# Performance work log

Hardware: AMD Instinct MI355X
Metric: run time of the kernel (lower is better)

## Reference

```python
import jax, jax.numpy as jnp
import numpy as np

N, F, E, A, H = 50000, 64, 1600000, 8, 16
RECEPTIVE_FIELD = 7


def setup_inputs() -> dict:
    key = jax.random.key(0)
    ks = jax.random.split(key, 12)
    inp = {
        "x": jax.random.normal(ks[0], (N, F), dtype=jnp.float32),
        "edge_index": jax.random.randint(ks[1], (2, E), 0, N, dtype=jnp.int64),
        "w1": jax.random.normal(ks[2], (F, H), dtype=jnp.float32) * 0.1,
        "b1": jax.random.normal(ks[3], (H,), dtype=jnp.float32) * 0.1,
        "w2": jax.random.normal(ks[4], (H, H), dtype=jnp.float32) * 0.1,
        "b2": jax.random.normal(ks[5], (H,), dtype=jnp.float32) * 0.1,
        "w3": jax.random.normal(ks[6], (H, F), dtype=jnp.float32) * 0.1,
        "b3": jax.random.normal(ks[7], (F,), dtype=jnp.float32) * 0.1,
        "fc1_w": jax.random.normal(ks[8], ((1 + RECEPTIVE_FIELD) * F, F), dtype=jnp.float32) * 0.05,
        "fc1_b": jax.random.normal(ks[9], (F,), dtype=jnp.float32) * 0.05,
        "fc2_w": jax.random.normal(ks[10], (F, A), dtype=jnp.float32) * 0.1,
        "fc2_b": jax.random.normal(ks[11], (A,), dtype=jnp.float32) * 0.1,
    }
    return inp


def _mlp(x, w1, b1, w2, b2, w3, b3):
    h = jax.nn.relu(x @ w1 + b1)
    h = jax.nn.relu(h @ w2 + b2)
    return h @ w3 + b3


def _agg_mean(x, src, dst):
    # scatter-mean: mean of source-node features over incoming edges per target
    s = jax.ops.segment_sum(x[src], dst, num_segments=N)          # [N, F]
    cnt = jax.ops.segment_sum(jnp.ones((src.shape[0], 1), x.dtype), dst, num_segments=N)
    return s / jnp.maximum(cnt, 1.0)  # nodes with no in-edges -> 0 (torch mean aggr)


def reference(x, edge_index, w1, b1, w2, b2, w3, b3, fc1_w, fc1_b, fc2_w, fc2_b):
    src, dst = edge_index[0], edge_index[1]
    mlp = lambda t: _mlp(t, w1, b1, w2, b2, w3, b3)
    fields = [mlp(mlp(x))]
    for i in range(RECEPTIVE_FIELD):
        x_ = mlp(x)
        for _ in range(i + 1):
            x_ = _agg_mean(x_, src, dst)
        fields.append(mlp(x_))
    f = jnp.concatenate(fields, axis=1)          # [N, 8*F]
    h = f @ fc1_w + fc1_b                        # [N, F]
    logits = h @ fc2_w + fc2_b                   # [N, A]
    return jax.nn.softmax(logits, axis=-1)       # Categorical probs
```

## Files before the change

kernel.cpp:

```cpp
#include <hip/hip_runtime.h>


#define NB2MAX 400
#define NBLK   256
#define CAP2   32
#define CAPC   48
#define CAPB   6144
#define OVCAP  1024
#define LCAP   6144
#define CAPN   64

__global__ __launch_bounds__(1024) void binfill_k(
    const int* __restrict__ src, const int* __restrict__ dst, int E, int n,
    int* __restrict__ gcur, int* __restrict__ ovbuf,
    int* __restrict__ bins, int* __restrict__ cnts,
    const float* __restrict__ w1, const float* __restrict__ w3,
    const float* __restrict__ b3, const float* __restrict__ fc1w,
    const float* __restrict__ fc1b, const float* __restrict__ fc2w,
    const float* __restrict__ fc2b,
    float* __restrict__ M, float* __restrict__ cvec,
    float* __restrict__ W31, float* __restrict__ c31) {
    __shared__ int lbuf[NB2MAX * CAP2];
    __shared__ int lcnt[NB2MAX];
    __shared__ int lflush[NB2MAX];
    int tid = threadIdx.x;
    int NB = (n + 127) >> 7;

    if ((int)blockIdx.x >= NBLK) {
        float* fl = (float*)lbuf;
        int s = (int)blockIdx.x - NBLK;
        if (s == 0) {
            if (tid < 256) {
                int i = tid >> 4, j = tid & 15;
                float a = 0.f;
                for (int g = 0; g < 64; g++) a += w3[i * 64 + g] * w1[g * 16 + j];
                W31[tid] = a;
            } else if (tid < 272) {
                int j = tid - 256;
                float a = 0.f;
                for (int g = 0; g < 64; g++) a += b3[g] * w1[g * 16 + j];
                c31[j] = a;
            } else if (tid >= 320 && tid < 384) {
                int h = tid - 320;
                float a = 0.f;
                for (int r = 0; r < 512; r++) a += b3[r & 63] * fc1w[r * 64 + h];
                fl[h] = a;
            }
            __syncthreads();
            if (tid < 8) {
                float a = fc2b[tid];
                for (int h = 0; h < 64; h++) a += (fc1b[h] + fl[h]) * fc2w[h * 8 + tid];
                cvec[tid] = a;
            }
        } else {
            int k = s - 1;
            {
                int i = tid >> 6, h = tid & 63;
                float a = 0.f;
                const float* f1 = fc1w + (size_t)(k * 64) * 64 + h;
                for (int g = 0; g < 64; g++) a += w3[i * 64 + g] * f1[g * 64];
                fl[i * 64 + h] = a;
            }
            __syncthreads();
            if (tid < 128) {
                int i = tid >> 3, j = tid & 7;
                float a = 0.f;
                for (int h = 0; h < 64; h++) a += fl[i * 64 + h] * fc2w[h * 8 + j];
                M[k * 128 + i * 8 + j] = a;
            }
        }
        return;
    }

    for (int b = tid; b < NB; b += 1024) { lcnt[b] = 0; lflush[b] = 0; }
    __syncthreads();
    int blk = blockIdx.x;
    int chunk = (E + NBLK - 1) / NBLK;
    int beg = blk * chunk;
    int end = beg + chunk; if (end > E) end = E;
    for (int t0 = beg; t0 < end; t0 += 1024) {
        int e = t0 + tid;
        if (e < end) {
            int d = dst[e], s = src[e];
            if ((unsigned)d < (unsigned)n && (unsigned)s < (unsigned)n) {
                int b = d >> 7;
                int pk = ((d & 127) << 16) | s;
                int pos = atomicAdd(&lcnt[b], 1);
                if (pos < CAP2) lbuf[b * CAP2 + pos] = pk;
                else {
                    int p = atomicAdd(&gcur[b], 1);
                    if (p < OVCAP) ovbuf[b * OVCAP + p] = pk;
                }
            }
        }
        __syncthreads();
        for (int b = tid; b < NB; b += 1024) {
            int cnt = lcnt[b]; if (cnt > CAP2) cnt = CAP2;
            int fl2 = lflush[b];
            size_t cell = ((size_t)b * NBLK + blk) * CAPC;
            int base = 0;
            while (cnt - base >= 16) {
                if (fl2 + 16 <= CAPC) {
                    int* dp = bins + cell + fl2;
                    #pragma unroll
                    for (int q = 0; q < 16; q++) dp[q] = lbuf[b * CAP2 + base + q];
                    fl2 += 16;
                } else {
                    int p = atomicAdd(&gcur[b], 16);
                    for (int q = 0; q < 16; q++)
                        if (p + q < OVCAP) ovbuf[b * OVCAP + p + q] = lbuf[b * CAP2 + base + q];
                }
                base += 16;
            }
            int rem = cnt - base;
            if (base > 0)
                for (int q = 0; q < rem; q++) lbuf[b * CAP2 + q] = lbuf[b * CAP2 + base + q];
            lcnt[b] = rem; lflush[b] = fl2;
        }
        __syncthreads();
    }
    for (int b = tid; b < NB; b += 1024) {
        int cnt = lcnt[b]; if (cnt > CAP2) cnt = CAP2;
        int fl2 = lflush[b];
        size_t cell = ((size_t)b * NBLK + blk) * CAPC;
        if (fl2 + cnt <= CAPC) {
            for (int q = 0; q < cnt; q++) bins[cell + fl2 + q] = lbuf[b * CAP2 + q];
            fl2 += cnt;
        } else {
            int p = atomicAdd(&gcur[b], cnt);
            for (int q = 0; q < cnt; q++)
                if (p + q < OVCAP) ovbuf[b * OVCAP + p + q] = lbuf[b * CAP2 + q];
        }
        cnts[(size_t)blk * NB + b] = fl2;
    }
}

__global__ __launch_bounds__(256) void csr2_k(
    const int* __restrict__ bins, const int* __restrict__ cnts,
    const int* __restrict__ gcur, const int* __restrict__ ovbuf,
    unsigned short* __restrict__ csrp, int* __restrict__ degs,
    int* __restrict__ csr, int2* __restrict__ be,
    int* __restrict__ lists, int* __restrict__ lcnt3, int n) {
    __shared__ int hist[128], pref[128], cur[128];
    __shared__ int scnt[NBLK];
    __shared__ int lbuf[LCAP];
    __shared__ int sov;
    __shared__ int ccnt[3], cbase[3];
    int tid = threadIdx.x;
    int NB = (n + 127) >> 7;
    int b = blockIdx.x;
    if (tid < 128) { hist[tid] = 0; cur[tid] = 0; }
    if (tid < 3) ccnt[tid] = 0;
    scnt[tid] = cnts[(size_t)tid * NB + b];
    if (tid == 0) {
        int g = gcur[b];
        sov = g < 0 ? 0 : (g > OVCAP ? OVCAP : g);
    }
    __syncthreads();
    {
        int c = scnt[tid];
        size_t cell = ((size_t)b * NBLK + tid) * CAPC;
        for (int i = 0; i < c; i++) atomicAdd(&hist[bins[cell + i] >> 16], 1);
    }
    if (tid == 0)
        for (int i = 0; i < sov; i++) atomicAdd(&hist[ovbuf[b * OVCAP + i] >> 16], 1);
    __syncthreads();
    if (tid == 0) {
        int r = 0;
        for (int i = 0; i < 128; i++) { pref[i] = r; r += hist[i]; }
    }
    __syncthreads();
    {
        int c = scnt[tid];
        size_t cell = ((size_t)b * NBLK + tid) * CAPC;
        for (int i = 0; i < c; i++) {
            int pk = bins[cell + i];
            int dl = pk >> 16;
            int pos = pref[dl] + atomicAdd(&cur[dl], 1);
            if (pos < LCAP) lbuf[pos] = pk & 0xffff;
        }
    }
    if (tid == 0) {
        for (int i = 0; i < sov; i++) {
            int pk = ovbuf[b * OVCAP + i];
            int dl = pk >> 16;
            int pos = pref[dl] + atomicAdd(&cur[dl], 1);
            if (pos < LCAP) lbuf[pos] = pk & 0xffff;
        }
    }
    __syncthreads();
    for (int q = tid; q < 128 * CAPN; q += 256) {
        int dl = q >> 6, j = q & 63;
        int d = (b << 7) + dl;
        if (d >= n) break;
        int cnt = hist[dl];
        int v = (j < cnt) ? lbuf[pref[dl] + j] : n;
        int pos = ((j & 3) << 4) | (j >> 2);
        csrp[(size_t)d * CAPN + pos] = (unsigned short)v;
    }
    int myc = -1, lpos = 0;
    if (tid < 128) {
        int d = (b << 7) + tid;
        if (d < n) {
            int cnt = hist[tid];
            degs[d] = cnt;
            myc = cnt <= 32 ? 0 : (cnt <= 48 ? 1 : 2);
            lpos = atomicAdd(&ccnt[myc], 1);
            if (cnt > CAPN) {
                int s0 = b * CAPB + pref[tid];
                be[d] = make_int2(s0 + CAPN, s0 + cnt);
                for (int j = CAPN; j < cnt; j++)
                    csr[s0 + j] = lbuf[pref[tid] + j] << 2;
            }
        }
    }
    __syncthreads();
    if (tid < 3) cbase[tid] = atomicAdd(&lcnt3[tid], ccnt[tid]);
    __syncthreads();
    if (myc >= 0) lists[(size_t)myc * n + cbase[myc] + lpos] = (b << 7) + tid;
}

__global__ __launch_bounds__(256) void proj_k(
    const float* __restrict__ x, float* __restrict__ z0, float* __restrict__ z1,
    float* __restrict__ logits,
    const float* __restrict__ w1, const float* __restrict__ b1,
    const float* __restrict__ w2, const float* __restrict__ b2,
    const float* __restrict__ W31, const float* __restrict__ c31,
    const float* __restrict__ M0, const float* __restrict__ cvec, int n) {
    __shared__ float sw1[1024], sw2[256], sW[256], sM[128];
    __shared__ float sb1[16], sb2[16], sc[16], scv[8];
    int tid = threadIdx.x;
    for (int i = tid; i < 1024; i += 256) sw1[i] = w1[i];
    sw2[tid] = w2[tid & 255];
    sW[tid & 255] = W31[tid & 255];
    if (tid < 128) sM[tid] = M0[tid];
    if (tid < 16) { sb1[tid] = b1[tid]; sb2[tid] = b2[tid]; sc[tid] = c31[tid]; }
    if (tid < 8) scv[tid] = cvec[tid];
    __syncthreads();
    if (blockIdx.x == 0 && tid < 16) {
        z0[(size_t)n * 16 + tid] = 0.f;
        z1[(size_t)n * 16 + tid] = 0.f;
    }
    int nid = blockIdx.x * 256 + tid;
    if (nid >= n) return;
    float t1[16];
    #pragma unroll
    for (int j = 0; j < 16; j++) t1[j] = sb1[j];
    const float4* xp = (const float4*)(x + (size_t)nid * 64);
    #pragma unroll
    for (int q = 0; q < 16; q++) {
        float4 v = xp[q];
        #pragma unroll
        for (int j = 0; j < 16; j++)
            t1[j] += v.x * sw1[(4 * q) * 16 + j] + v.y * sw1[(4 * q + 1) * 16 + j]
                   + v.z * sw1[(4 * q + 2) * 16 + j] + v.w * sw1[(4 * q + 3) * 16 + j];
    }
    #pragma unroll
    for (int j = 0; j < 16; j++) t1[j] = fmaxf(t1[j], 0.f);
    float t2[16];
    #pragma unroll
    for (int j = 0; j < 16; j++) {
        float a = sb2[j];
        #pragma unroll
        for (int i = 0; i < 16; i++) a += t1[i] * sw2[i * 16 + j];
        t2[j] = fmaxf(a, 0.f);
    }
    float z[16];
    #pragma unroll
    for (int j = 0; j < 16; j++) {
        float a = sc[j];
        #pragma unroll
        for (int i = 0; i < 16; i++) a += t2[i] * sW[i * 16 + j];
        z[j] = a;
    }
    float4* zo = (float4*)(z0 + (size_t)nid * 16);
    #pragma unroll
    for (int q = 0; q < 4; q++)
        zo[q] = make_float4(z[4 * q], z[4 * q + 1], z[4 * q + 2], z[4 * q + 3]);
    float h[16], f2[16];
    #pragma unroll
    for (int i = 0; i < 16; i++) h[i] = fmaxf(z[i] + sb1[i], 0.f);
    #pragma unroll
    for (int j = 0; j < 16; j++) {
        float a = sb2[j];
        #pragma unroll
        for (int i = 0; i < 16; i++) a += h[i] * sw2[i * 16 + j];
        f2[j] = fmaxf(a, 0.f);
    }
    float* lp = logits + (size_t)nid * 8;
    #pragma unroll
    for (int j = 0; j < 8; j++) {
        float l = scv[j];
        #pragma unroll
        for (int i = 0; i < 16; i++) l += f2[i] * sM[i * 8 + j];
        lp[j] = l;
    }
}

__global__ __launch_bounds__(256, 4) void hop_k(
    const float* __restrict__ zin, float* __restrict__ zout, float* __restrict__ logits,
    const unsigned short* __restrict__ csrp, const int* __restrict__ degs,
    const int2* __restrict__ be, const int* __restrict__ csr,
    const int* __restrict__ lists, const int* __restrict__ lcnt3,
    const float* __restrict__ w2, const float* __restrict__ b1,
    const float* __restrict__ b2, const float* __restrict__ M, int n, int FB) {
    __shared__ float sw2[256], sM[128], sb1[16], sb2[16];
    int tid = threadIdx.x;
    if ((int)blockIdx.x < FB) {
        sw2[tid] = w2[tid];
        if (tid < 128) sM[tid] = M[tid];
        if (tid < 16) { sb1[tid] = b1[tid]; sb2[tid] = b2[tid]; }
        __syncthreads();
        int nid = blockIdx.x * 256 + tid;
        if (nid >= n) return;
        float h[16];
        const float4* zp = (const float4*)(zin + (size_t)nid * 16);
        #pragma unroll
        for (int q = 0; q < 4; q++) {
            float4 v = zp[q];
            h[4 * q] = v.x; h[4 * q + 1] = v.y; h[4 * q + 2] = v.z; h[4 * q + 3] = v.w;
        }
        #pragma unroll
        for (int i = 0; i < 16; i++) h[i] = fmaxf(h[i] + sb1[i], 0.f);
        float t2[16];
        #pragma unroll
        for (int j = 0; j < 16; j++) {
            float a = sb2[j];
            #pragma unroll
            for (int i = 0; i < 16; i++) a += h[i] * sw2[i * 16 + j];
            t2[j] = fmaxf(a, 0.f);
        }
        float* lp = logits + (size_t)nid * 8;
        #pragma unroll
        for (int j = 0; j < 8; j++) {
            float l = 0.f;
            #pragma unroll
            for (int i = 0; i < 16; i++) l += t2[i] * sM[i * 8 + j];
            lp[j] += l;
        }
        return;
    }
    int wave = tid >> 6;
    int lane = tid & 63;
    int quarter = lane >> 4;
    int l16 = lane & 15;
    int t = l16 >> 2, c = l16 & 3;
    int idx = (((int)blockIdx.x - FB) * 4 + wave) * 4 + quarter;
    if (idx >= n) return;
    int ns = lcnt3[0];
    int nm = lcnt3[1];
    int tier, node;
    if (idx < ns)           { tier = 0; node = lists[idx]; }
    else if (idx < ns + nm) { tier = 1; node = lists[(size_t)n + (idx - ns)]; }
    else                    { tier = 2; node = lists[2 * (size_t)n + (idx - ns - nm)]; }
    int degi = degs[node];
    const uint4* ip = (const uint4*)(csrp + ((size_t)node << 6));
    uint4 pa = ip[t * 2];
    int r0 = pa.x & 0xffff, r1 = pa.x >> 16;
    int r2 = pa.y & 0xffff, r3 = pa.y >> 16;
    int r4 = pa.z & 0xffff, r5 = pa.z >> 16;
    int r6 = pa.w & 0xffff, r7 = pa.w >> 16;
    const float4* z4 = (const float4*)zin;
    float4 v0 = z4[((size_t)r0 << 2) + c];
    float4 v1 = z4[((size_t)r1 << 2) + c];
    float4 v2 = z4[((size_t)r2 << 2) + c];
    float4 v3 = z4[((size_t)r3 << 2) + c];
    float4 v4 = z4[((size_t)r4 << 2) + c];
    float4 v5 = z4[((size_t)r5 << 2) + c];
    float4 v6 = z4[((size_t)r6 << 2) + c];
    float4 v7 = z4[((size_t)r7 << 2) + c];
    float ax = ((v0.x + v1.x) + (v2.x + v3.x)) + ((v4.x + v5.x) + (v6.x + v7.x));
    float ay = ((v0.y + v1.y) + (v2.y + v3.y)) + ((v4.y + v5.y) + (v6.y + v7.y));
    float az = ((v0.z + v1.z) + (v2.z + v3.z)) + ((v4.z + v5.z) + (v6.z + v7.z));
    float aw = ((v0.w + v1.w) + (v2.w + v3.w)) + ((v4.w + v5.w) + (v6.w + v7.w));
    if (tier >= 1) {
        uint4 pb = ip[t * 2 + 1];
        int r8 = pb.x & 0xffff, r9 = pb.x >> 16;
        int rA = pb.y & 0xffff, rB = pb.y >> 16;
        float4 v8 = z4[((size_t)r8 << 2) + c];
        float4 v9 = z4[((size_t)r9 << 2) + c];
        float4 vA = z4[((size_t)rA << 2) + c];
        float4 vB = z4[((size_t)rB << 2) + c];
        ax += (v8.x + v9.x) + (vA.x + vB.x);
        ay += (v8.y + v9.y) + (vA.y + vB.y);
        az += (v8.z + v9.z) + (vA.z + vB.z);
        aw += (v8.w + v9.w) + (vA.w + vB.w);
        if (tier == 2) {
            int rC = pb.z & 0xffff, rD = pb.z >> 16;
            int rE = pb.w & 0xffff, rF = pb.w >> 16;
            float4 vC = z4[((size_t)rC << 2) + c];
            float4 vD = z4[((size_t)rD << 2) + c];
            float4 vE = z4[((size_t)rE << 2) + c];
            float4 vF = z4[((size_t)rF << 2) + c];
            ax += (vC.x + vD.x) + (vE.x + vF.x);
            ay += (vC.y + vD.y) + (vE.y + vF.y);
            az += (vC.z + vD.z) + (vE.z + vF.z);
            aw += (vC.w + vD.w) + (vE.w + vF.w);
            if (degi > CAPN) {
                int2 r = be[node];
                for (int q = r.x + t; q < r.y; q += 4) {
                    float4 v = z4[(size_t)csr[q] + c];
                    ax += v.x; ay += v.y; az += v.z; aw += v.w;
                }
            }
        }
    }
    #pragma unroll
    for (int off = 8; off >= 4; off >>= 1) {
        ax += __shfl_down(ax, off, 16);
        ay += __shfl_down(ay, off, 16);
        az += __shfl_down(az, off, 16);
        aw += __shfl_down(aw, off, 16);
    }
    if (l16 < 4) {
        float inv = 1.f / (float)(degi > 0 ? degi : 1);
        ((float4*)(zout + (size_t)node * 16))[l16] =
            make_float4(ax * inv, ay * inv, az * inv, aw * inv);
    }
}

__global__ __launch_bounds__(256) void fieldsoft_k(
    const float* __restrict__ z, float* __restrict__ logits,
    const float* __restrict__ w2, const float* __restrict__ b1,
    const float* __restrict__ b2, const float* __restrict__ M, int n) {
    __shared__ float sw2[256], sM[128], sb1[16], sb2[16];
    int tid = threadIdx.x;
    sw2[tid] = w2[tid];
    if (tid < 128) sM[tid] = M[tid];
    if (tid < 16) { sb1[tid] = b1[tid]; sb2[tid] = b2[tid]; }
    __syncthreads();
    int nid = blockIdx.x * 256 + tid;
    if (nid >= n) return;
    float h[16];
    const float4* zp = (const float4*)(z + (size_t)nid * 16);
    #pragma unroll
    for (int q = 0; q < 4; q++) {
        float4 v = zp[q];
        h[4 * q] = v.x; h[4 * q + 1] = v.y; h[4 * q + 2] = v.z; h[4 * q + 3] = v.w;
    }
    #pragma unroll
    for (int i = 0; i < 16; i++) h[i] = fmaxf(h[i] + sb1[i], 0.f);
    float t2[16];
    #pragma unroll
    for (int j = 0; j < 16; j++) {
        float a = sb2[j];
        #pragma unroll
        for (int i = 0; i < 16; i++) a += h[i] * sw2[i * 16 + j];
        t2[j] = fmaxf(a, 0.f);
    }
    float4* lp4 = (float4*)(logits + (size_t)nid * 8);
    float4 l0 = lp4[0], l1 = lp4[1];
    float v[8] = {l0.x, l0.y, l0.z, l0.w, l1.x, l1.y, l1.z, l1.w};
    #pragma unroll
    for (int j = 0; j < 8; j++) {
        float l = 0.f;
        #pragma unroll
        for (int i = 0; i < 16; i++) l += t2[i] * sM[i * 8 + j];
        v[j] += l;
    }
    float m = v[0];
    #pragma unroll
    for (int j = 1; j < 8; j++) m = fmaxf(m, v[j]);
    float s = 0.f;
    #pragma unroll
    for (int j = 0; j < 8; j++) { v[j] = expf(v[j] - m); s += v[j]; }
    float inv = 1.f / s;
    lp4[0] = make_float4(v[0] * inv, v[1] * inv, v[2] * inv, v[3] * inv);
    lp4[1] = make_float4(v[4] * inv, v[5] * inv, v[6] * inv, v[7] * inv);
}

extern "C" void kernel_launch(void* const* d_in, const int* in_sizes, int n_in,
                              void* d_out, int out_size, void* d_ws, size_t ws_size,
                              hipStream_t stream) {
    const float* x    = (const float*)d_in[0];
    const int*   ei   = (const int*)d_in[1];
    const float* w1   = (const float*)d_in[2];
    const float* b1   = (const float*)d_in[3];
    const float* w2   = (const float*)d_in[4];
    const float* b2   = (const float*)d_in[5];
    const float* w3   = (const float*)d_in[6];
    const float* b3   = (const float*)d_in[7];
    const float* fc1w = (const float*)d_in[8];
    const float* fc1b = (const float*)d_in[9];
    const float* fc2w = (const float*)d_in[10];
    const float* fc2b = (const float*)d_in[11];
    float* out = (float*)d_out;

    int n = in_sizes[0] / 64;
    int E = in_sizes[1] / 2;
    int NB = (n + 127) >> 7;
    const int* src = ei;
    const int* dst = ei + E;

    char* ws = (char*)d_ws;
    auto carve = [&](size_t bytes) {
        char* p = ws;
        ws += (bytes + 255) & ~((size_t)255);
        return p;
    };
    int*   gcur    = (int*)carve((size_t)NB * 4);
    int*   lcnt3   = (int*)carve(16);
    int*   ovbuf   = (int*)carve((size_t)NB * OVCAP * 4);
    int*   binsbuf = (int*)carve((size_t)NB * NBLK * CAPC * 4);
    int*   cnts    = (int*)carve((size_t)NBLK * NB * 4);
    unsigned short* csrp = (unsigned short*)carve((size_t)n * CAPN * 2);
    int*   degs    = (int*)carve((size_t)n * 4);
    int*   csr     = (int*)carve((size_t)NB * CAPB * 4);
    int2*  be      = (int2*)carve((size_t)n * 8);
    int*   lists   = (int*)carve((size_t)3 * n * 4);
    float* buf0    = (float*)carve((size_t)(n + 1) * 16 * 4);
    float* buf1    = (float*)carve((size_t)(n + 1) * 16 * 4);
    float* M       = (float*)carve(1024 * 4);
    float* cvec    = (float*)carve(8 * 4);
    float* W31     = (float*)carve(256 * 4);
    float* c31     = (float*)carve(16 * 4);

    size_t gpad = ((size_t)NB * 4 + 255) & ~((size_t)255);
    hipMemsetAsync(gcur, 0, gpad + 16, stream);
    binfill_k<<<NBLK + 9, 1024, 0, stream>>>(src, dst, E, n, gcur, ovbuf, binsbuf, cnts,
                                             w1, w3, b3, fc1w, fc1b, fc2w, fc2b,
                                             M, cvec, W31, c31);

    int FB = (n + 255) / 256;
    int AB = (n + 15) / 16;
    csr2_k<<<NB, 256, 0, stream>>>(binsbuf, cnts, gcur, ovbuf, csrp, degs, csr, be,
                                   lists, lcnt3, n);
    proj_k<<<FB, 256, 0, stream>>>(x, buf0, buf1, out, w1, b1, w2, b2,
                                   W31, c31, M, cvec, n);

    float* cur = buf0;
    float* nxt = buf1;
    hop_k<<<AB, 256, 0, stream>>>(cur, nxt, out, csrp, degs, be, csr, lists, lcnt3,
                                  w2, b1, b2, M, n, 0);
    { float* t = cur; cur = nxt; nxt = t; }
    for (int k = 1; k <= 6; k++) {
        hop_k<<<FB + AB, 256, 0, stream>>>(cur, nxt, out, csrp, degs, be, csr,
                                           lists, lcnt3,
                                           w2, b1, b2, M + k * 128, n, FB);
        float* t = cur; cur = nxt; nxt = t;
    }
    fieldsoft_k<<<FB, 256, 0, stream>>>(cur, out, w2, b1, b2, M + 7 * 128, n);
}
```

Before: 255.2 us.

## Fuse projection and seven aggregation hops into one cooperative persistent kernel

Replaces the projection kernel, the seven hop launches and the final field-softmax kernel with a single cooperative kernel of 512 blocks. Grid-wide syncs separate the hops, and each thread keeps its node's logits in registers until the final softmax, so the per-hop read-modify-write of logits in global memory goes away. The aim is to cut launch overhead and logits traffic. The cost is a fixed small grid with low occupancy for the latency-bound gathers, plus per-hop serialization of aggregation and MLP work that the separate launches could partly overlap. It falls back to the old multi-kernel path when the stream is being captured or the cooperative launch fails.

```diff
diff --git a/kernel.cpp b/kernel.cpp
--- a/kernel.cpp
+++ b/kernel.cpp
@@ -1,4 +1,7 @@
 #include <hip/hip_runtime.h>
+#include <hip/hip_cooperative_groups.h>
+
+namespace cg = cooperative_groups;
 
 
 #define NB2MAX 400
@@ -9,6 +12,7 @@
 #define OVCAP  1024
 #define LCAP   6144
 #define CAPN   64
+#define PGRID  512
 
 __global__ __launch_bounds__(1024) void binfill_k(
     const int* __restrict__ src, const int* __restrict__ dst, int E, int n,
@@ -220,6 +224,226 @@
     if (myc >= 0) lists[(size_t)myc * n + cbase[myc] + lpos] = (b << 7) + tid;
 }
 
+__device__ __forceinline__ void agg_one(
+    int idx, int ns, int nm, int n, int t4, int ch, int l16,
+    const float4* __restrict__ z4, float* __restrict__ zo,
+    const unsigned short* __restrict__ csrp, const int* __restrict__ degs,
+    const int2* __restrict__ be, const int* __restrict__ csr,
+    const int* __restrict__ lists) {
+    int tier, node;
+    if (idx < ns)           { tier = 0; node = lists[idx]; }
+    else if (idx < ns + nm) { tier = 1; node = lists[(size_t)n + (idx - ns)]; }
+    else                    { tier = 2; node = lists[2 * (size_t)n + (idx - ns - nm)]; }
+    int degi = degs[node];
+    const uint4* ip = (const uint4*)(csrp + ((size_t)node << 6));
+    uint4 pa = ip[t4 * 2];
+    int r0 = pa.x & 0xffff, r1 = pa.x >> 16;
+    int r2 = pa.y & 0xffff, r3 = pa.y >> 16;
+    int r4 = pa.z & 0xffff, r5 = pa.z >> 16;
+    int r6 = pa.w & 0xffff, r7 = pa.w >> 16;
+    float4 v0 = z4[((size_t)r0 << 2) + ch];
+    float4 v1 = z4[((size_t)r1 << 2) + ch];
+    float4 v2 = z4[((size_t)r2 << 2) + ch];
+    float4 v3 = z4[((size_t)r3 << 2) + ch];
+    float4 v4 = z4[((size_t)r4 << 2) + ch];
+    float4 v5 = z4[((size_t)r5 << 2) + ch];
+    float4 v6 = z4[((size_t)r6 << 2) + ch];
+    float4 v7 = z4[((size_t)r7 << 2) + ch];
+    float ax = ((v0.x + v1.x) + (v2.x + v3.x)) + ((v4.x + v5.x) + (v6.x + v7.x));
+    float ay = ((v0.y + v1.y) + (v2.y + v3.y)) + ((v4.y + v5.y) + (v6.y + v7.y));
+    float az = ((v0.z + v1.z) + (v2.z + v3.z)) + ((v4.z + v5.z) + (v6.z + v7.z));
+    float aw = ((v0.w + v1.w) + (v2.w + v3.w)) + ((v4.w + v5.w) + (v6.w + v7.w));
+    if (tier >= 1) {
+        uint4 pb = ip[t4 * 2 + 1];
+        int r8 = pb.x & 0xffff, r9 = pb.x >> 16;
+        int rA = pb.y & 0xffff, rB = pb.y >> 16;
+        float4 v8 = z4[((size_t)r8 << 2) + ch];
+        float4 v9 = z4[((size_t)r9 << 2) + ch];
+        float4 vA = z4[((size_t)rA << 2) + ch];
+        float4 vB = z4[((size_t)rB << 2) + ch];
+        ax += (v8.x + v9.x) + (vA.x + vB.x);
+        ay += (v8.y + v9.y) + (vA.y + vB.y);
+        az += (v8.z + v9.z) + (vA.z + vB.z);
+        aw += (v8.w + v9.w) + (vA.w + vB.w);
+        if (tier == 2) {
+            int rC = pb.z & 0xffff, rD = pb.z >> 16;
+            int rE = pb.w & 0xffff, rF = pb.w >> 16;
+            float4 vC = z4[((size_t)rC << 2) + ch];
+            float4 vD = z4[((size_t)rD << 2) + ch];
+            float4 vE = z4[((size_t)rE << 2) + ch];
+            float4 vF = z4[((size_t)rF << 2) + ch];
+            ax += (vC.x + vD.x) + (vE.x + vF.x);
+            ay += (vC.y + vD.y) + (vE.y + vF.y);
+            az += (vC.z + vD.z) + (vE.z + vF.z);
+            aw += (vC.w + vD.w) + (vE.w + vF.w);
+            if (degi > CAPN) {
+                int2 r = be[node];
+                for (int q = r.x + t4; q < r.y; q += 4) {
+                    float4 v = z4[(size_t)csr[q] + ch];
+                    ax += v.x; ay += v.y; az += v.z; aw += v.w;
+                }
+            }
+        }
+    }
+    #pragma unroll
+    for (int off = 8; off >= 4; off >>= 1) {
+        ax += __shfl_down(ax, off, 16);
+        ay += __shfl_down(ay, off, 16);
+        az += __shfl_down(az, off, 16);
+        aw += __shfl_down(aw, off, 16);
+    }
+    if (l16 < 4) {
+        float inv = 1.f / (float)(degi > 0 ? degi : 1);
+        ((float4*)(zo + (size_t)node * 16))[l16] =
+            make_float4(ax * inv, ay * inv, az * inv, aw * inv);
+    }
+}
+
+__global__ __launch_bounds__(256, 2) void fused_k(
+    const float* __restrict__ x,
+    float* __restrict__ bufA, float* __restrict__ bufB,
+    float* __restrict__ out,
+    const unsigned short* __restrict__ csrp, const int* __restrict__ degs,
+    const int2* __restrict__ be, const int* __restrict__ csr,
+    const int* __restrict__ lists, const int* __restrict__ lcnt3,
+    const float* __restrict__ w1, const float* __restrict__ b1,
+    const float* __restrict__ w2, const float* __restrict__ b2,
+    const float* __restrict__ W31, const float* __restrict__ c31,
+    const float* __restrict__ M, const float* __restrict__ cvec, int n) {
+    cg::grid_group grid = cg::this_grid();
+    __shared__ float sw1[1024], sM[1024], sw2[256], sW[256];
+    __shared__ float sb1[16], sb2[16], sc[16], scv[8];
+    int tid = threadIdx.x;
+    for (int i = tid; i < 1024; i += 256) { sw1[i] = w1[i]; sM[i] = M[i]; }
+    sw2[tid] = w2[tid];
+    sW[tid] = W31[tid];
+    if (tid < 16) { sb1[tid] = b1[tid]; sb2[tid] = b2[tid]; sc[tid] = c31[tid]; }
+    if (tid < 8) scv[tid] = cvec[tid];
+    __syncthreads();
+
+    int gtid = (int)blockIdx.x * 256 + tid;
+    float lg[8];
+    #pragma unroll
+    for (int j = 0; j < 8; j++) lg[j] = 0.f;
+
+    if (blockIdx.x == 0 && tid < 16) {
+        bufA[(size_t)n * 16 + tid] = 0.f;
+        bufB[(size_t)n * 16 + tid] = 0.f;
+    }
+    if (gtid < n) {
+        float t1[16];
+        #pragma unroll
+        for (int j = 0; j < 16; j++) t1[j] = sb1[j];
+        const float4* xp = (const float4*)(x + (size_t)gtid * 64);
+        #pragma unroll
+        for (int q = 0; q < 16; q++) {
+            float4 v = xp[q];
+            #pragma unroll
+            for (int j = 0; j < 16; j++)
+                t1[j] += v.x * sw1[(4 * q) * 16 + j] + v.y * sw1[(4 * q + 1) * 16 + j]
+                       + v.z * sw1[(4 * q + 2) * 16 + j] + v.w * sw1[(4 * q + 3) * 16 + j];
+        }
+        #pragma unroll
+        for (int j = 0; j < 16; j++) t1[j] = fmaxf(t1[j], 0.f);
+        float t2[16];
+        #pragma unroll
+        for (int j = 0; j < 16; j++) {
+            float a = sb2[j];
+            #pragma unroll
+            for (int i = 0; i < 16; i++) a += t1[i] * sw2[i * 16 + j];
+            t2[j] = fmaxf(a, 0.f);
+        }
+        float z[16];
+        #pragma unroll
+        for (int j = 0; j < 16; j++) {
+            float a = sc[j];
+            #pragma unroll
+            for (int i = 0; i < 16; i++) a += t2[i] * sW[i * 16 + j];
+            z[j] = a;
+        }
+        float4* zo4 = (float4*)(bufA + (size_t)gtid * 16);
+        #pragma unroll
+        for (int q = 0; q < 4; q++)
+            zo4[q] = make_float4(z[4 * q], z[4 * q + 1], z[4 * q + 2], z[4 * q + 3]);
+        float h[16], f2[16];
+        #pragma unroll
+        for (int i = 0; i < 16; i++) h[i] = fmaxf(z[i] + sb1[i], 0.f);
+        #pragma unroll
+        for (int j = 0; j < 16; j++) {
+            float a = sb2[j];
+            #pragma unroll
+            for (int i = 0; i < 16; i++) a += h[i] * sw2[i * 16 + j];
+            f2[j] = fmaxf(a, 0.f);
+        }
+        #pragma unroll
+        for (int j = 0; j < 8; j++) {
+            float l = scv[j];
+            #pragma unroll
+            for (int i = 0; i < 16; i++) l += f2[i] * sM[i * 8 + j];
+            lg[j] = l;
+        }
+    }
+    __threadfence(); grid.sync(); __threadfence();
+
+    int wid = (int)blockIdx.x * 4 + (tid >> 6);
+    int lane = tid & 63;
+    int quarter = lane >> 4;
+    int l16 = lane & 15;
+    int t4 = l16 >> 2, ch = l16 & 3;
+    int ns = lcnt3[0], nm = lcnt3[1];
+
+    const float* zi = bufA;
+    float* zo = bufB;
+    for (int k = 1; k <= 7; k++) {
+        const float4* z4 = (const float4*)zi;
+        for (int idx = wid * 4 + quarter; idx < n; idx += PGRID * 16)
+            agg_one(idx, ns, nm, n, t4, ch, l16, z4, zo,
+                    csrp, degs, be, csr, lists);
+        __threadfence(); grid.sync(); __threadfence();
+        if (gtid < n) {
+            float h[16];
+            const float4* zp = (const float4*)(zo + (size_t)gtid * 16);
+            #pragma unroll
+            for (int q = 0; q < 4; q++) {
+                float4 v = zp[q];
+                h[4 * q] = v.x; h[4 * q + 1] = v.y; h[4 * q + 2] = v.z; h[4 * q + 3] = v.w;
+            }
+            #pragma unroll
+            for (int i = 0; i < 16; i++) h[i] = fmaxf(h[i] + sb1[i], 0.f);
+            float t2[16];
+            #pragma unroll
+            for (int j = 0; j < 16; j++) {
+                float a = sb2[j];
+                #pragma unroll
+                for (int i = 0; i < 16; i++) a += h[i] * sw2[i * 16 + j];
+                t2[j] = fmaxf(a, 0.f);
+            }
+            const float* Mk = sM + k * 128;
+            #pragma unroll
+            for (int j = 0; j < 8; j++) {
+                float l = 0.f;
+                #pragma unroll
+                for (int i = 0; i < 16; i++) l += t2[i] * Mk[i * 8 + j];
+                lg[j] += l;
+            }
+        }
+        const float* ts = zi; zi = zo; zo = (float*)ts;
+    }
+
+    if (gtid < n) {
+        float m = lg[0];
+        #pragma unroll
+        for (int j = 1; j < 8; j++) m = fmaxf(m, lg[j]);
+        float s = 0.f;
+        #pragma unroll
+        for (int j = 0; j < 8; j++) { lg[j] = expf(lg[j] - m); s += lg[j]; }
+        float inv = 1.f / s;
+        float4* lp4 = (float4*)(out + (size_t)gtid * 8);
+        lp4[0] = make_float4(lg[0] * inv, lg[1] * inv, lg[2] * inv, lg[3] * inv);
+        lp4[1] = make_float4(lg[4] * inv, lg[5] * inv, lg[6] * inv, lg[7] * inv);
+    }
+}
+
 __global__ __launch_bounds__(256) void proj_k(
     const float* __restrict__ x, float* __restrict__ z0, float* __restrict__ z1,
     float* __restrict__ logits,
@@ -344,79 +568,12 @@
     int lane = tid & 63;
     int quarter = lane >> 4;
     int l16 = lane & 15;
-    int t = l16 >> 2, c = l16 & 3;
+    int t4 = l16 >> 2, ch = l16 & 3;
     int idx = (((int)blockIdx.x - FB) * 4 + wave) * 4 + quarter;
     if (idx >= n) return;
-    int ns = lcnt3[0];
-    int nm = lcnt3[1];
-    int tier, node;
-    if (idx < ns)           { tier = 0; node = lists[idx]; }
-    else if (idx < ns + nm) { tier = 1; node = lists[(size_t)n + (idx - ns)]; }
-    else                    { tier = 2; node = lists[2 * (size_t)n + (idx - ns - nm)]; }
-    int degi = degs[node];
-    const uint4* ip = (const uint4*)(csrp + ((size_t)node << 6));
-    uint4 pa = ip[t * 2];
-    int r0 = pa.x & 0xffff, r1 = pa.x >> 16;
-    int r2 = pa.y & 0xffff, r3 = pa.y >> 16;
-    int r4 = pa.z & 0xffff, r5 = pa.z >> 16;
-    int r6 = pa.w & 0xffff, r7 = pa.w >> 16;
-    const float4* z4 = (const float4*)zin;
-    float4 v0 = z4[((size_t)r0 << 2) + c];
-    float4 v1 = z4[((size_t)r1 << 2) + c];
-    float4 v2 = z4[((size_t)r2 << 2) + c];
-    float4 v3 = z4[((size_t)r3 << 2) + c];
-    float4 v4 = z4[((size_t)r4 << 2) + c];
-    float4 v5 = z4[((size_t)r5 << 2) + c];
-    float4 v6 = z4[((size_t)r6 << 2) + c];
-    float4 v7 = z4[((size_t)r7 << 2) + c];
-    float ax = ((v0.x + v1.x) + (v2.x + v3.x)) + ((v4.x + v5.x) + (v6.x + v7.x));
-    float ay = ((v0.y + v1.y) + (v2.y + v3.y)) + ((v4.y + v5.y) + (v6.y + v7.y));
-    float az = ((v0.z + v1.z) + (v2.z + v3.z)) + ((v4.z + v5.z) + (v6.z + v7.z));
-    float aw = ((v0.w + v1.w) + (v2.w + v3.w)) + ((v4.w + v5.w) + (v6.w + v7.w));
-    if (tier >= 1) {
-        uint4 pb = ip[t * 2 + 1];
-        int r8 = pb.x & 0xffff, r9 = pb.x >> 16;
-        int rA = pb.y & 0xffff, rB = pb.y >> 16;
-        float4 v8 = z4[((size_t)r8 << 2) + c];
-        float4 v9 = z4[((size_t)r9 << 2) + c];
-        float4 vA = z4[((size_t)rA << 2) + c];
-        float4 vB = z4[((size_t)rB << 2) + c];
-        ax += (v8.x + v9.x) + (vA.x + vB.x);
-        ay += (v8.y + v9.y) + (vA.y + vB.y);
-        az += (v8.z + v9.z) + (vA.z + vB.z);
-        aw += (v8.w + v9.w) + (vA.w + vB.w);
-        if (tier == 2) {
-            int rC = pb.z & 0xffff, rD = pb.z >> 16;
-            int rE = pb.w & 0xffff, rF = pb.w >> 16;
-            float4 vC = z4[((size_t)rC << 2) + c];
-            float4 vD = z4[((size_t)rD << 2) + c];
-            float4 vE = z4[((size_t)rE << 2) + c];
-            float4 vF = z4[((size_t)rF << 2) + c];
-            ax += (vC.x + vD.x) + (vE.x + vF.x);
-            ay += (vC.y + vD.y) + (vE.y + vF.y);
-            az += (vC.z + vD.z) + (vE.z + vF.z);
-            aw += (vC.w + vD.w) + (vE.w + vF.w);
-            if (degi > CAPN) {
-                int2 r = be[node];
-                for (int q = r.x + t; q < r.y; q += 4) {
-                    float4 v = z4[(size_t)csr[q] + c];
-                    ax += v.x; ay += v.y; az += v.z; aw += v.w;
-                }
-            }
-        }
-    }
-    #pragma unroll
-    for (int off = 8; off >= 4; off >>= 1) {
-        ax += __shfl_down(ax, off, 16);
-        ay += __shfl_down(ay, off, 16);
-        az += __shfl_down(az, off, 16);
-        aw += __shfl_down(aw, off, 16);
-    }
-    if (l16 < 4) {
-        float inv = 1.f / (float)(degi > 0 ? degi : 1);
-        ((float4*)(zout + (size_t)node * 16))[l16] =
-            make_float4(ax * inv, ay * inv, az * inv, aw * inv);
-    }
+    int ns = lcnt3[0], nm = lcnt3[1];
+    agg_one(idx, ns, nm, n, t4, ch, l16, (const float4*)zin, zout,
+            csrp, degs, be, csr, lists);
 }
 
 __global__ __launch_bounds__(256) void fieldsoft_k(
@@ -520,24 +677,40 @@
     binfill_k<<<NBLK + 9, 1024, 0, stream>>>(src, dst, E, n, gcur, ovbuf, binsbuf, cnts,
                                              w1, w3, b3, fc1w, fc1b, fc2w, fc2b,
                                              M, cvec, W31, c31);
-
-    int FB = (n + 255) / 256;
-    int AB = (n + 15) / 16;
     csr2_k<<<NB, 256, 0, stream>>>(binsbuf, cnts, gcur, ovbuf, csrp, degs, csr, be,
                                    lists, lcnt3, n);
-    proj_k<<<FB, 256, 0, stream>>>(x, buf0, buf1, out, w1, b1, w2, b2,
-                                   W31, c31, M, cvec, n);
-
-    float* cur = buf0;
-    float* nxt = buf1;
-    hop_k<<<AB, 256, 0, stream>>>(cur, nxt, out, csrp, degs, be, csr, lists, lcnt3,
-                                  w2, b1, b2, M, n, 0);
-    { float* t = cur; cur = nxt; nxt = t; }
-    for (int k = 1; k <= 6; k++) {
-        hop_k<<<FB + AB, 256, 0, stream>>>(cur, nxt, out, csrp, degs, be, csr,
-                                           lists, lcnt3,
-                                           w2, b1, b2, M + k * 128, n, FB);
-        float* t = cur; cur = nxt; nxt = t;
-    }
-    fieldsoft_k<<<FB, 256, 0, stream>>>(cur, out, w2, b1, b2, M + 7 * 128, n);
+
+    bool coop_ok = false;
+    hipStreamCaptureStatus cap = hipStreamCaptureStatusNone;
+    (void)hipStreamIsCapturing(stream, &cap);
+    if (cap == hipStreamCaptureStatusNone) {
+        void* kargs[] = {
+            (void*)&x, (void*)&buf0, (void*)&buf1, (void*)&out,
+            (void*)&csrp, (void*)&degs, (void*)&be, (void*)&csr,
+            (void*)&lists, (void*)&lcnt3,
+            (void*)&w1, (void*)&b1, (void*)&w2, (void*)&b2,
+            (void*)&W31, (void*)&c31, (void*)&M, (void*)&cvec, (void*)&n
+        };
+        hipError_t err = hipLaunchCooperativeKernel((void*)fused_k, dim3(PGRID),
+                                                    dim3(256), kargs, 0, stream);
+        coop_ok = (err == hipSuccess);
+    }
+    if (!coop_ok) {
+        int FB = (n + 255) / 256;
+        int AB = (n + 15) / 16;
+        proj_k<<<FB, 256, 0, stream>>>(x, buf0, buf1, out, w1, b1, w2, b2,
+                                       W31, c31, M, cvec, n);
+        float* cur = buf0;
+        float* nxt = buf1;
+        hop_k<<<AB, 256, 0, stream>>>(cur, nxt, out, csrp, degs, be, csr,
+                                      lists, lcnt3, w2, b1, b2, M, n, 0);
+        { float* t = cur; cur = nxt; nxt = t; }
+        for (int k = 1; k <= 6; k++) {
+            hop_k<<<FB + AB, 256, 0, stream>>>(cur, nxt, out, csrp, degs, be, csr,
+                                               lists, lcnt3,
+                                               w2, b1, b2, M + k * 128, n, FB);
+            float* t = cur; cur = nxt; nxt = t;
+        }
+        fieldsoft_k<<<FB, 256, 0, stream>>>(cur, out, w2, b1, b2, M + 7 * 128, n);
+    }
 }
```

New measurement: 254.3 us. No clear change (-0.4%).

## Fuse CSR build with projection and store adjacency in tier-sorted order

Applied to the files above, without the earlier changes.

The CSR-construction kernel and the projection kernel are merged into one launch, with separate block ranges for each job, so the two independent stages can overlap. The padded adjacency rows and (node, degree) pairs are now written directly at their tier-sorted slot. Each hop kernel then reads them sequentially by index instead of going through a lists array plus a degs lookup. This removes one indirection and one launch per pass, at the cost of a larger slot-indexed buffer (3*n rows) and a fused kernel whose shared-memory footprint is the larger of the two branches.

```diff
diff --git a/kernel.cpp b/kernel.cpp
--- a/kernel.cpp
+++ b/kernel.cpp
@@ -135,77 +135,85 @@
     }
 }
 
-__global__ __launch_bounds__(256) void csr2_k(
+__global__ __launch_bounds__(256) void csr2p_k(
     const int* __restrict__ bins, const int* __restrict__ cnts,
     const int* __restrict__ gcur, const int* __restrict__ ovbuf,
-    unsigned short* __restrict__ csrp, int* __restrict__ degs,
-    int* __restrict__ csr, int2* __restrict__ be,
-    int* __restrict__ lists, int* __restrict__ lcnt3, int n) {
-    __shared__ int hist[128], pref[128], cur[128];
-    __shared__ int scnt[NBLK];
-    __shared__ int lbuf[LCAP];
-    __shared__ int sov;
-    __shared__ int ccnt[3], cbase[3];
+    unsigned short* __restrict__ csrp_s, int2* __restrict__ nd_s,
+    int* __restrict__ csr, int2* __restrict__ be, int* __restrict__ lcnt3,
+    const float* __restrict__ x, float* __restrict__ z0, float* __restrict__ z1,
+    float* __restrict__ logits,
+    const float* __restrict__ w1, const float* __restrict__ b1,
+    const float* __restrict__ w2, const float* __restrict__ b2,
+    const float* __restrict__ W31, const float* __restrict__ c31,
+    const float* __restrict__ M0, const float* __restrict__ cvec,
+    int n, int NBARG) {
     int tid = threadIdx.x;
-    int NB = (n + 127) >> 7;
-    int b = blockIdx.x;
-    if (tid < 128) { hist[tid] = 0; cur[tid] = 0; }
-    if (tid < 3) ccnt[tid] = 0;
-    scnt[tid] = cnts[(size_t)tid * NB + b];
-    if (tid == 0) {
-        int g = gcur[b];
-        sov = g < 0 ? 0 : (g > OVCAP ? OVCAP : g);
-    }
-    __syncthreads();
-    {
-        int c = scnt[tid];
-        size_t cell = ((size_t)b * NBLK + tid) * CAPC;
-        for (int i = 0; i < c; i++) atomicAdd(&hist[bins[cell + i] >> 16], 1);
-    }
-    if (tid == 0)
-        for (int i = 0; i < sov; i++) atomicAdd(&hist[ovbuf[b * OVCAP + i] >> 16], 1);
-    __syncthreads();
-    if (tid == 0) {
-        int r = 0;
-        for (int i = 0; i < 128; i++) { pref[i] = r; r += hist[i]; }
-    }
-    __syncthreads();
-    {
-        int c = scnt[tid];
-        size_t cell = ((size_t)b * NBLK + tid) * CAPC;
-        for (int i = 0; i < c; i++) {
-            int pk = bins[cell + i];
-            int dl = pk >> 16;
-            int pos = pref[dl] + atomicAdd(&cur[dl], 1);
-            if (pos < LCAP) lbuf[pos] = pk & 0xffff;
-        }
-    }
-    if (tid == 0) {
-        for (int i = 0; i < sov; i++) {
-            int pk = ovbuf[b * OVCAP + i];
-            int dl = pk >> 16;
-            int pos = pref[dl] + atomicAdd(&cur[dl], 1);
-            if (pos < LCAP) lbuf[pos] = pk & 0xffff;
-        }
-    }
-    __syncthreads();
-    for (int q = tid; q < 128 * CAPN; q += 256) {
-        int dl = q >> 6, j = q & 63;
-        int d = (b << 7) + dl;
-        if (d >= n) break;
-        int cnt = hist[dl];
-        int v = (j < cnt) ? lbuf[pref[dl] + j] : n;
-        int pos = ((j & 3) << 4) | (j >> 2);
-        csrp[(size_t)d * CAPN + pos] = (unsigned short)v;
-    }
-    int myc = -1, lpos = 0;
-    if (tid < 128) {
-        int d = (b << 7) + tid;
-        if (d < n) {
+    if ((int)blockIdx.x < NBARG) {
+        __shared__ int hist[128], pref[128], cur[128], slot[128];
+        __shared__ int scnt[NBLK];
+        __shared__ int lbuf[LCAP];
+        __shared__ int sov;
+        __shared__ int ccnt[3], cbase[3];
+        int NB = (n + 127) >> 7;
+        int b = blockIdx.x;
+        if (tid < 128) { hist[tid] = 0; cur[tid] = 0; }
+        if (tid < 3) ccnt[tid] = 0;
+        scnt[tid] = cnts[(size_t)tid * NB + b];
+        if (tid == 0) {
+            int g = gcur[b];
+            sov = g < 0 ? 0 : (g > OVCAP ? OVCAP : g);
+        }
+        __syncthreads();
+        {
+            int c = scnt[tid];
+            size_t cell = ((size_t)b * NBLK + tid) * CAPC;
+            for (int i = 0; i < c; i++) atomicAdd(&hist[bins[cell + i] >> 16], 1);
+        }
+        if (tid == 0)
+            for (int i = 0; i < sov; i++) atomicAdd(&hist[ovbuf[b * OVCAP + i] >> 16], 1);
+        __syncthreads();
+        if (tid == 0) {
+            int r = 0;
+            for (int i = 0; i < 128; i++) { pref[i] = r; r += hist[i]; }
+        }
+        __syncthreads();
+        {
+            int c = scnt[tid];
+            size_t cell = ((size_t)b * NBLK + tid) * CAPC;
+            for (int i = 0; i < c; i++) {
+                int pk = bins[cell + i];
+                int dl = pk >> 16;
+                int pos = pref[dl] + atomicAdd(&cur[dl], 1);
+                if (pos < LCAP) lbuf[pos] = pk & 0xffff;
+            }
+        }
+        if (tid == 0) {
+            for (int i = 0; i < sov; i++) {
+                int pk = ovbuf[b * OVCAP + i];
+                int dl = pk >> 16;
+                int pos = pref[dl] + atomicAdd(&cur[dl], 1);
+                if (pos < LCAP) lbuf[pos] = pk & 0xffff;
+            }
+        }
+        __syncthreads();
+        int myc = -1, lpos = 0;
+        if (tid < 128) {
+            int d = (b << 7) + tid;
+            if (d < n) {
+                int cnt = hist[tid];
+                myc = cnt <= 32 ? 0 : (cnt <= 48 ? 1 : 2);
+                lpos = atomicAdd(&ccnt[myc], 1);
+            }
+        }
+        __syncthreads();
+        if (tid < 3) cbase[tid] = atomicAdd(&lcnt3[tid], ccnt[tid]);
+        __syncthreads();
+        if (myc >= 0) {
+            int d = (b << 7) + tid;
             int cnt = hist[tid];
-            degs[d] = cnt;
-            myc = cnt <= 32 ? 0 : (cnt <= 48 ? 1 : 2);
-            lpos = atomicAdd(&ccnt[myc], 1);
+            int s = myc * n + cbase[myc] + lpos;
+            slot[tid] = s;
+            nd_s[s] = make_int2(d, cnt);
             if (cnt > CAPN) {
                 int s0 = b * CAPB + pref[tid];
                 be[d] = make_int2(s0 + CAPN, s0 + cnt);
@@ -213,23 +221,20 @@
                     csr[s0 + j] = lbuf[pref[tid] + j] << 2;
             }
         }
-    }
-    __syncthreads();
-    if (tid < 3) cbase[tid] = atomicAdd(&lcnt3[tid], ccnt[tid]);
-    __syncthreads();
-    if (myc >= 0) lists[(size_t)myc * n + cbase[myc] + lpos] = (b << 7) + tid;
-}
-
-__global__ __launch_bounds__(256) void proj_k(
-    const float* __restrict__ x, float* __restrict__ z0, float* __restrict__ z1,
-    float* __restrict__ logits,
-    const float* __restrict__ w1, const float* __restrict__ b1,
-    const float* __restrict__ w2, const float* __restrict__ b2,
-    const float* __restrict__ W31, const float* __restrict__ c31,
-    const float* __restrict__ M0, const float* __restrict__ cvec, int n) {
+        __syncthreads();
+        for (int q = tid; q < 128 * CAPN; q += 256) {
+            int dl = q >> 6, j = q & 63;
+            int d = (b << 7) + dl;
+            if (d >= n) break;
+            int cnt = hist[dl];
+            int v = (j < cnt) ? lbuf[pref[dl] + j] : n;
+            int pos = ((j & 3) << 4) | (j >> 2);
+            csrp_s[(size_t)slot[dl] * CAPN + pos] = (unsigned short)v;
+        }
+        return;
+    }
     __shared__ float sw1[1024], sw2[256], sW[256], sM[128];
     __shared__ float sb1[16], sb2[16], sc[16], scv[8];
-    int tid = threadIdx.x;
     for (int i = tid; i < 1024; i += 256) sw1[i] = w1[i];
     sw2[tid] = w2[tid & 255];
     sW[tid & 255] = W31[tid & 255];
@@ -237,11 +242,11 @@
     if (tid < 16) { sb1[tid] = b1[tid]; sb2[tid] = b2[tid]; sc[tid] = c31[tid]; }
     if (tid < 8) scv[tid] = cvec[tid];
     __syncthreads();
-    if (blockIdx.x == 0 && tid < 16) {
+    if ((int)blockIdx.x == NBARG && tid < 16) {
         z0[(size_t)n * 16 + tid] = 0.f;
         z1[(size_t)n * 16 + tid] = 0.f;
     }
-    int nid = blockIdx.x * 256 + tid;
+    int nid = ((int)blockIdx.x - NBARG) * 256 + tid;
     if (nid >= n) return;
     float t1[16];
     #pragma unroll
@@ -299,9 +304,9 @@
 
 __global__ __launch_bounds__(256, 4) void hop_k(
     const float* __restrict__ zin, float* __restrict__ zout, float* __restrict__ logits,
-    const unsigned short* __restrict__ csrp, const int* __restrict__ degs,
+    const unsigned short* __restrict__ csrp_s, const int2* __restrict__ nd_s,
     const int2* __restrict__ be, const int* __restrict__ csr,
-    const int* __restrict__ lists, const int* __restrict__ lcnt3,
+    const int* __restrict__ lcnt3,
     const float* __restrict__ w2, const float* __restrict__ b1,
     const float* __restrict__ b2, const float* __restrict__ M, int n, int FB) {
     __shared__ float sw2[256], sM[128], sb1[16], sb2[16];
@@ -344,43 +349,43 @@
     int lane = tid & 63;
     int quarter = lane >> 4;
     int l16 = lane & 15;
-    int t = l16 >> 2, c = l16 & 3;
+    int t4 = l16 >> 2, ch = l16 & 3;
     int idx = (((int)blockIdx.x - FB) * 4 + wave) * 4 + quarter;
     if (idx >= n) return;
-    int ns = lcnt3[0];
-    int nm = lcnt3[1];
-    int tier, node;
-    if (idx < ns)           { tier = 0; node = lists[idx]; }
-    else if (idx < ns + nm) { tier = 1; node = lists[(size_t)n + (idx - ns)]; }
-    else                    { tier = 2; node = lists[2 * (size_t)n + (idx - ns - nm)]; }
-    int degi = degs[node];
-    const uint4* ip = (const uint4*)(csrp + ((size_t)node << 6));
-    uint4 pa = ip[t * 2];
+    int ns = lcnt3[0], nm = lcnt3[1];
+    int tier; size_t row;
+    if (idx < ns)           { tier = 0; row = (size_t)idx; }
+    else if (idx < ns + nm) { tier = 1; row = (size_t)n + (idx - ns); }
+    else                    { tier = 2; row = 2 * (size_t)n + (idx - ns - nm); }
+    int2 nd = nd_s[row];
+    int node = nd.x, degi = nd.y;
+    const uint4* ip = (const uint4*)(csrp_s + (row << 6));
+    uint4 pa = ip[t4 * 2];
     int r0 = pa.x & 0xffff, r1 = pa.x >> 16;
     int r2 = pa.y & 0xffff, r3 = pa.y >> 16;
     int r4 = pa.z & 0xffff, r5 = pa.z >> 16;
     int r6 = pa.w & 0xffff, r7 = pa.w >> 16;
     const float4* z4 = (const float4*)zin;
-    float4 v0 = z4[((size_t)r0 << 2) + c];
-    float4 v1 = z4[((size_t)r1 << 2) + c];
-    float4 v2 = z4[((size_t)r2 << 2) + c];
-    float4 v3 = z4[((size_t)r3 << 2) + c];
-    float4 v4 = z4[((size_t)r4 << 2) + c];
-    float4 v5 = z4[((size_t)r5 << 2) + c];
-    float4 v6 = z4[((size_t)r6 << 2) + c];
-    float4 v7 = z4[((size_t)r7 << 2) + c];
+    float4 v0 = z4[((size_t)r0 << 2) + ch];
+    float4 v1 = z4[((size_t)r1 << 2) + ch];
+    float4 v2 = z4[((size_t)r2 << 2) + ch];
+    float4 v3 = z4[((size_t)r3 << 2) + ch];
+    float4 v4 = z4[((size_t)r4 << 2) + ch];
+    float4 v5 = z4[((size_t)r5 << 2) + ch];
+    float4 v6 = z4[((size_t)r6 << 2) + ch];
+    float4 v7 = z4[((size_t)r7 << 2) + ch];
     float ax = ((v0.x + v1.x) + (v2.x + v3.x)) + ((v4.x + v5.x) + (v6.x + v7.x));
     float ay = ((v0.y + v1.y) + (v2.y + v3.y)) + ((v4.y + v5.y) + (v6.y + v7.y));
     float az = ((v0.z + v1.z) + (v2.z + v3.z)) + ((v4.z + v5.z) + (v6.z + v7.z));
     float aw = ((v0.w + v1.w) + (v2.w + v3.w)) + ((v4.w + v5.w) + (v6.w + v7.w));
     if (tier >= 1) {
-        uint4 pb = ip[t * 2 + 1];
+        uint4 pb = ip[t4 * 2 + 1];
         int r8 = pb.x & 0xffff, r9 = pb.x >> 16;
         int rA = pb.y & 0xffff, rB = pb.y >> 16;
-        float4 v8 = z4[((size_t)r8 << 2) + c];
-        float4 v9 = z4[((size_t)r9 << 2) + c];
-        float4 vA = z4[((size_t)rA << 2) + c];
-        float4 vB = z4[((size_t)rB << 2) + c];
+        float4 v8 = z4[((size_t)r8 << 2) + ch];
+        float4 v9 = z4[((size_t)r9 << 2) + ch];
+        float4 vA = z4[((size_t)rA << 2) + ch];
+        float4 vB = z4[((size_t)rB << 2) + ch];
         ax += (v8.x + v9.x) + (vA.x + vB.x);
         ay += (v8.y + v9.y) + (vA.y + vB.y);
         az += (v8.z + v9.z) + (vA.z + vB.z);
@@ -388,18 +393,18 @@
         if (tier == 2) {
             int rC = pb.z & 0xffff, rD = pb.z >> 16;
             int rE = pb.w & 0xffff, rF = pb.w >> 16;
-            float4 vC = z4[((size_t)rC << 2) + c];
-            float4 vD = z4[((size_t)rD << 2) + c];
-            float4 vE = z4[((size_t)rE << 2) + c];
-            float4 vF = z4[((size_t)rF << 2) + c];
+            float4 vC = z4[((size_t)rC << 2) + ch];
+            float4 vD = z4[((size_t)rD << 2) + ch];
+            float4 vE = z4[((size_t)rE << 2) + ch];
+            float4 vF = z4[((size_t)rF << 2) + ch];
             ax += (vC.x + vD.x) + (vE.x + vF.x);
             ay += (vC.y + vD.y) + (vE.y + vF.y);
             az += (vC.z + vD.z) + (vE.z + vF.z);
             aw += (vC.w + vD.w) + (vE.w + vF.w);
             if (degi > CAPN) {
                 int2 r = be[node];
-                for (int q = r.x + t; q < r.y; q += 4) {
-                    float4 v = z4[(size_t)csr[q] + c];
+                for (int q = r.x + t4; q < r.y; q += 4) {
+                    float4 v = z4[(size_t)csr[q] + ch];
                     ax += v.x; ay += v.y; az += v.z; aw += v.w;
                 }
             }
@@ -503,11 +508,10 @@
     int*   ovbuf   = (int*)carve((size_t)NB * OVCAP * 4);
     int*   binsbuf = (int*)carve((size_t)NB * NBLK * CAPC * 4);
     int*   cnts    = (int*)carve((size_t)NBLK * NB * 4);
-    unsigned short* csrp = (unsigned short*)carve((size_t)n * CAPN * 2);
-    int*   degs    = (int*)carve((size_t)n * 4);
+    unsigned short* csrp_s = (unsigned short*)carve((size_t)3 * n * CAPN * 2);
+    int2*  nd_s    = (int2*)carve((size_t)3 * n * 8);
     int*   csr     = (int*)carve((size_t)NB * CAPB * 4);
     int2*  be      = (int2*)carve((size_t)n * 8);
-    int*   lists   = (int*)carve((size_t)3 * n * 4);
     float* buf0    = (float*)carve((size_t)(n + 1) * 16 * 4);
     float* buf1    = (float*)carve((size_t)(n + 1) * 16 * 4);
     float* M       = (float*)carve(1024 * 4);
@@ -523,20 +527,19 @@
 
     int FB = (n + 255) / 256;
     int AB = (n + 15) / 16;
-    csr2_k<<<NB, 256, 0, stream>>>(binsbuf, cnts, gcur, ovbuf, csrp, degs, csr, be,
-                                   lists, lcnt3, n);
-    proj_k<<<FB, 256, 0, stream>>>(x, buf0, buf1, out, w1, b1, w2, b2,
-                                   W31, c31, M, cvec, n);
+    csr2p_k<<<NB + FB, 256, 0, stream>>>(binsbuf, cnts, gcur, ovbuf,
+                                         csrp_s, nd_s, csr, be, lcnt3,
+                                         x, buf0, buf1, out, w1, b1, w2, b2,
+                                         W31, c31, M, cvec, n, NB);
 
     float* cur = buf0;
     float* nxt = buf1;
-    hop_k<<<AB, 256, 0, stream>>>(cur, nxt, out, csrp, degs, be, csr, lists, lcnt3,
+    hop_k<<<AB, 256, 0, stream>>>(cur, nxt, out, csrp_s, nd_s, be, csr, lcnt3,
                                   w2, b1, b2, M, n, 0);
     { float* t = cur; cur = nxt; nxt = t; }
     for (int k = 1; k <= 6; k++) {
-        hop_k<<<FB + AB, 256, 0, stream>>>(cur, nxt, out, csrp, degs, be, csr,
-                                           lists, lcnt3,
-                                           w2, b1, b2, M + k * 128, n, FB);
+        hop_k<<<FB + AB, 256, 0, stream>>>(cur, nxt, out, csrp_s, nd_s, be, csr,
+                                           lcnt3, w2, b1, b2, M + k * 128, n, FB);
         float* t = cur; cur = nxt; nxt = t;
     }
     fieldsoft_k<<<FB, 256, 0, stream>>>(cur, out, w2, b1, b2, M + 7 * 128, n);
```

Result: slower. 260.8 us (+2.2%).
